# Optimization experiments

Measured on AMD Instinct MI355X. Metric: run time of the kernel, lower is better.

## Reference

```python
import jax, jax.numpy as jnp
import numpy as np

NUM_HEADS = 4
NUM_GROUPS = 8
EPS = 1e-5


def group_norm(x, w, b):
    # x: [B, C, H, W], 8 groups, per-channel affine
    B, C, H, W = x.shape
    g = x.reshape(B, NUM_GROUPS, C // NUM_GROUPS, H, W)
    mu = g.mean(axis=(2, 3, 4), keepdims=True)
    var = g.var(axis=(2, 3, 4), keepdims=True)
    g = (g - mu) * jax.lax.rsqrt(var + EPS)
    x = g.reshape(B, C, H, W)
    return x * w[None, :, None, None] + b[None, :, None, None]


def setup_inputs() -> dict:
    key = jax.random.key(0)
    ks = jax.random.split(key, 7)
    B, C, H, W = 16, 256, 32, 32
    x = jax.random.normal(ks[0], (B, C, H, W), dtype=jnp.float32)
    norm_w = jnp.ones((C,), jnp.float32)
    norm_b = jnp.zeros((C,), jnp.float32)
    # 1x1 convs == channel matmuls; fan-in scaled init
    qkv_w = jax.random.normal(ks[1], (3 * C, C), dtype=jnp.float32) / np.sqrt(C)
    qkv_b = jnp.zeros((3 * C,), jnp.float32)
    proj_w = jax.random.normal(ks[2], (C, C), dtype=jnp.float32) / np.sqrt(C)
    proj_b = jnp.zeros((C,), jnp.float32)
    return {"x": x, "norm_w": norm_w, "norm_b": norm_b,
            "qkv_w": qkv_w, "qkv_b": qkv_b,
            "proj_w": proj_w, "proj_b": proj_b}


def reference(x, norm_w, norm_b, qkv_w, qkv_b, proj_w, proj_b):
    B, C, H, W = x.shape
    nh = NUM_HEADS
    d = C // nh
    N = H * W

    h = group_norm(x, norm_w, norm_b)
    # 1x1 conv -> channel matmul: [B, 3C, H, W]
    qkv = jnp.einsum('oc,bchw->bohw', qkv_w, h) + qkv_b[None, :, None, None]
    qkv = qkv.reshape(B, 3, nh, d, N)
    q, k, v = qkv[:, 0], qkv[:, 1], qkv[:, 2]  # [B, nh, d, N]

    scale = d ** (-0.5)
    attn = jnp.einsum('bhcn,bhcm->bhnm', q, k) * scale  # [B, nh, N, N]
    attn = jax.nn.softmax(attn, axis=-1)
    out = jnp.einsum('bhnm,bhcm->bhcn', attn, v)  # [B, nh, d, N]
    out = out.reshape(B, C, H, W)
    out = jnp.einsum('oc,bchw->bohw', proj_w, out) + proj_b[None, :, None, None]
    return x + out
```

## Files before the change

kernel.cpp:

```cpp
#include <hip/hip_runtime.h>
#include <math.h>

#define BATCH 16
#define CH 256
#define NG 8
#define NH 4
#define HD 64
#define NN 1024
#define GSZ 32
#define GELEMS (GSZ * NN)

typedef __attribute__((ext_vector_type(8))) __bf16 bf16x8;
typedef __attribute__((ext_vector_type(4))) __bf16 bf16x4;
typedef __attribute__((ext_vector_type(4))) _Float16 f16x4;
typedef __attribute__((ext_vector_type(4))) float f32x4;

__device__ __forceinline__ unsigned short f2b(float f) {
    union { __bf16 h; unsigned short u; } c; c.h = (__bf16)f; return c.u;
}
__device__ __forceinline__ unsigned short f2h(float f) {
    union { _Float16 h; unsigned short u; } c; c.h = (_Float16)f; return c.u;
}

#define MFMA(a, b, c) __builtin_amdgcn_mfma_f32_16x16x32_bf16(a, b, c, 0, 0, 0)
#define MFMA16(a, b, c) __builtin_amdgcn_mfma_f32_16x16x16f16(a, b, c, 0, 0, 0)

__global__ __launch_bounds__(256) void prep_kernel(
    const float* __restrict__ x, const float* __restrict__ qkv_w,
    const float* __restrict__ proj_w, float* __restrict__ stats,
    unsigned short* __restrict__ wq, unsigned short* __restrict__ wp)
{
    int tid = threadIdx.x;
    if (blockIdx.x >= 128) {
        int t = (blockIdx.x - 128) * 256 + tid;
        const float* src; unsigned short* dst; size_t off;
        if (t < 24576) { src = qkv_w; dst = wq; off = (size_t)t * 8; }
        else           { src = proj_w; dst = wp; off = (size_t)(t - 24576) * 8; }
        const float4* s4 = (const float4*)(src + off);
        float4 a = s4[0], b = s4[1];
        bf16x8 pk;
        pk[0] = (__bf16)a.x; pk[1] = (__bf16)a.y; pk[2] = (__bf16)a.z; pk[3] = (__bf16)a.w;
        pk[4] = (__bf16)b.x; pk[5] = (__bf16)b.y; pk[6] = (__bf16)b.z; pk[7] = (__bf16)b.w;
        *(bf16x8*)(dst + off) = pk;
        return;
    }
    int b = blockIdx.x >> 3, g = blockIdx.x & 7;
    const float4* x4 = (const float4*)(x + ((size_t)b * CH + g * GSZ) * NN);
    float s = 0.f, ss = 0.f;
    #pragma unroll
    for (int i = 0; i < 32; ++i) {
        float4 v = x4[tid + i * 256];
        s  += v.x + v.y + v.z + v.w;
        ss += v.x * v.x + v.y * v.y + v.z * v.z + v.w * v.w;
    }
    #pragma unroll
    for (int off = 1; off < 64; off <<= 1) {
        s  += __shfl_xor(s, off);
        ss += __shfl_xor(ss, off);
    }
    __shared__ float red[8];
    int wave = tid >> 6, lane = tid & 63;
    if (lane == 0) { red[wave] = s; red[4 + wave] = ss; }
    __syncthreads();
    if (tid == 0) {
        float ts  = red[0] + red[1] + red[2] + red[3];
        float tss = red[4] + red[5] + red[6] + red[7];
        float mu  = ts * (1.f / GELEMS);
        float var = tss * (1.f / GELEMS) - mu * mu;
        stats[blockIdx.x * 2] = mu;
        stats[blockIdx.x * 2 + 1] = rsqrtf(var + 1e-5f);
    }
}

__global__ __launch_bounds__(256) void gn_apply_kernel(
    const float* __restrict__ x, const float* __restrict__ w,
    const float* __restrict__ bb, const float* __restrict__ stats,
    unsigned short* __restrict__ hT)
{
    __shared__ float Ts[64][68];
    __shared__ float wcp[256], bcp[256];
    const int b = blockIdx.y, n0 = blockIdx.x * 64;
    const int tid = threadIdx.x;
    {
        int c = tid, g = c >> 5;
        float mu = stats[(b * 8 + g) * 2], rs = stats[(b * 8 + g) * 2 + 1];
        float wc = w[c] * rs;
        wcp[c] = wc; bcp[c] = bb[c] - mu * wc;
    }
    __syncthreads();
    const float* xb = x + (size_t)b * CH * NN;
    const int c_l = tid >> 2, nq = tid & 3;
    const int n_l = tid >> 2, cq = tid & 3;
    for (int cb = 0; cb < 4; ++cb) {
        #pragma unroll
        for (int i = 0; i < 4; ++i)
            *(float4*)&Ts[c_l][nq * 4 + i * 16] =
                *(const float4*)(xb + (size_t)(cb * 64 + c_l) * NN + n0 + nq * 4 + i * 16);
        __syncthreads();
        #pragma unroll
        for (int s = 0; s < 2; ++s) {
            int cbase = cq * 16 + s * 8;
            bf16x8 pk;
            #pragma unroll
            for (int j = 0; j < 8; ++j) {
                int c = cb * 64 + cbase + j;
                pk[j] = (__bf16)(Ts[cbase + j][n_l] * wcp[c] + bcp[c]);
            }
            *(bf16x8*)(hT + ((size_t)b * NN + n0 + n_l) * CH + cb * 64 + cbase) = pk;
        }
        __syncthreads();
    }
}

template <int KIND>
__global__ __launch_bounds__(256) void gemm_kernel(
    const unsigned short* __restrict__ AT,
    const unsigned short* __restrict__ Wb,
    const float* __restrict__ bias,
    unsigned short* __restrict__ outT, unsigned short* __restrict__ outV,
    const float* __restrict__ res, float* __restrict__ out)
{
    __shared__ __align__(16) unsigned short Ws[64][136];
    __shared__ __align__(16) unsigned short Hs[64][136];
    const int b = blockIdx.z, o0 = blockIdx.y * 64, n0 = blockIdx.x * 64;
    const int tid = threadIdx.x;
    const int lane = tid & 63, wv = tid >> 6;
    const int l = lane & 15, quad = lane >> 4;
    const int iw = wv & 1, jw = wv >> 1;
    const bool qk_mode = (KIND == 0) && (blockIdx.y < 8);
    const bool v_mode  = (KIND == 0) && (blockIdx.y >= 8);
    const int r4 = tid >> 2, c4 = tid & 3;

    f32x4 acc[2][2] = {};
    for (int st = 0; st < 2; ++st) {
        const int cc0 = st * 128;
        #pragma unroll
        for (int i = 0; i < 4; ++i) {
            int ch = c4 + i * 4;
            *(bf16x8*)&Ws[r4][ch * 8] =
                *(const bf16x8*)(Wb + (size_t)(o0 + r4) * CH + cc0 + ch * 8);
            *(bf16x8*)&Hs[r4][ch * 8] =
                *(const bf16x8*)(AT + ((size_t)b * NN + n0 + r4) * CH + cc0 + ch * 8);
        }
        __syncthreads();
        #pragma unroll
        for (int kt = 0; kt < 4; ++kt) {
            bf16x8 af[2], bf[2];
            #pragma unroll
            for (int i = 0; i < 2; ++i)
                af[i] = *(const bf16x8*)&Hs[iw * 32 + i * 16 + l][kt * 32 + quad * 8];
            #pragma unroll
            for (int j = 0; j < 2; ++j)
                bf[j] = *(const bf16x8*)&Ws[jw * 32 + j * 16 + l][kt * 32 + quad * 8];
            #pragma unroll
            for (int i = 0; i < 2; ++i)
                #pragma unroll
                for (int j = 0; j < 2; ++j)
                    acc[i][j] = v_mode ? MFMA(af[i], bf[j], acc[i][j])
                                       : MFMA(bf[j], af[i], acc[i][j]);
        }
        __syncthreads();
    }

    unsigned short* Cs = (unsigned short*)Ws;
    if (qk_mode) {
        #pragma unroll
        for (int i = 0; i < 2; ++i)
            #pragma unroll
            for (int j = 0; j < 2; ++j) {
                int o_p = jw * 32 + j * 16 + quad * 4;
                int n_l = iw * 32 + i * 16 + l;
                bf16x4 pk;
                #pragma unroll
                for (int r = 0; r < 4; ++r)
                    pk[r] = (__bf16)(acc[i][j][r] + bias[o0 + o_p + r]);
                *(bf16x4*)&Cs[n_l * 72 + o_p] = pk;
            }
        __syncthreads();
        int rr = tid >> 2, ch = tid & 3;
        bf16x8 a0 = *(const bf16x8*)&Cs[rr * 72 + ch * 16];
        bf16x8 a1 = *(const bf16x8*)&Cs[rr * 72 + ch * 16 + 8];
        unsigned short* dst = outT + ((size_t)b * NN + n0 + rr) * 512 + o0 + ch * 16;
        *(bf16x8*)dst = a0;
        *(bf16x8*)(dst + 8) = a1;
    } else if (v_mode) {
        #pragma unroll
        for (int i = 0; i < 2; ++i)
            #pragma unroll
            for (int j = 0; j < 2; ++j) {
                int n_p = iw * 32 + i * 16 + quad * 4;
                int o_l = jw * 32 + j * 16 + l;
                float bs = bias[o0 + o_l];
                f16x4 pk;
                #pragma unroll
                for (int r = 0; r < 4; ++r)
                    pk[r] = (_Float16)(acc[i][j][r] + bs);
                *(f16x4*)&Cs[o_l * 72 + n_p] = pk;
            }
        __syncthreads();
        int rr = tid >> 2, ch = tid & 3;
        bf16x8 a0 = *(const bf16x8*)&Cs[rr * 72 + ch * 16];
        bf16x8 a1 = *(const bf16x8*)&Cs[rr * 72 + ch * 16 + 8];
        unsigned short* dst = outV + ((size_t)b * CH + (o0 + rr - 512)) * NN + n0 + ch * 16;
        *(bf16x8*)dst = a0;
        *(bf16x8*)(dst + 8) = a1;
    } else {
        #pragma unroll
        for (int i = 0; i < 2; ++i)
            #pragma unroll
            for (int j = 0; j < 2; ++j) {
                int o = o0 + jw * 32 + j * 16 + quad * 4;
                int n = n0 + iw * 32 + i * 16 + l;
                #pragma unroll
                for (int r = 0; r < 4; ++r) {
                    size_t idx = ((size_t)b * CH + o + r) * NN + n;
                    out[idx] = acc[i][j][r] + bias[o + r] + res[idx];
                }
            }
    }
}

__global__ __launch_bounds__(256, 3) void attn_kernel(
    const unsigned short* __restrict__ qkvT,
    const unsigned short* __restrict__ vbuf,
    unsigned short* __restrict__ ctxT)
{
    __shared__ __align__(16) unsigned short KV[2][8192];
    __shared__ float Lred[2][32];
    const int id = blockIdx.x;
    const int bh = id & 63, nt = id >> 6;
    const int b = bh >> 2, hh = bh & 3;
    const int n0 = nt * 64;
    const int tid = threadIdx.x;
    const int lane = tid & 63, w = tid >> 6;
    const int l = lane & 15, quad = lane >> 4;
    const int qx = w & 1, ky = w >> 1;
    const float KL2E = 0.125f * 1.44269504f;
    const int r4 = tid >> 2, c4 = tid & 3;

    bf16x8 qf[2][2];
    {
        const unsigned short* qp = qkvT + ((size_t)b * NN + n0 + 32 * qx + l) * 512 + hh * 64;
        #pragma unroll
        for (int ns = 0; ns < 2; ++ns)
            #pragma unroll
            for (int kt = 0; kt < 2; ++kt)
                qf[ns][kt] = *(const bf16x8*)(qp + (size_t)ns * 16 * 512 + kt * 32 + quad * 8);
    }

    const unsigned short* gk = qkvT + ((size_t)b * NN + r4) * 512 + 256 + hh * 64;
    const unsigned short* gv = vbuf + ((size_t)b * CH + hh * 64 + r4) * NN;
    const int p0 = (c4 ^ (r4 & 7)) * 8, p1 = ((c4 + 4) ^ (r4 & 7)) * 8;

    bf16x8 kpre0, kpre1, vpre0, vpre1;
    kpre0 = *(const bf16x8*)(gk + c4 * 8);
    kpre1 = *(const bf16x8*)(gk + (c4 + 4) * 8);
    vpre0 = *(const bf16x8*)(gv + c4 * 8);
    vpre1 = *(const bf16x8*)(gv + (c4 + 4) * 8);
    *(bf16x8*)&KV[0][r4 * 64 + p0] = kpre0;
    *(bf16x8*)&KV[0][r4 * 64 + p1] = kpre1;
    *(bf16x8*)&KV[0][4096 + r4 * 64 + p0] = vpre0;
    *(bf16x8*)&KV[0][4096 + r4 * 64 + p1] = vpre1;
    __syncthreads();

    float l_w[2] = {0.f, 0.f};
    f32x4 oacc[2][4] = {};

    for (int mt = 0; mt < 16; ++mt) {
        const int cur = mt & 1;
        if (mt < 15) {
            const unsigned short* gk1 = gk + (size_t)(mt + 1) * 64 * 512;
            const unsigned short* gv1 = gv + (mt + 1) * 64;
            kpre0 = *(const bf16x8*)(gk1 + c4 * 8);
            kpre1 = *(const bf16x8*)(gk1 + (c4 + 4) * 8);
            vpre0 = *(const bf16x8*)(gv1 + c4 * 8);
            vpre1 = *(const bf16x8*)(gv1 + (c4 + 4) * 8);
        }

        bf16x8 kf[2][2];
        #pragma unroll
        for (int mt2 = 0; mt2 < 2; ++mt2)
            #pragma unroll
            for (int kt = 0; kt < 2; ++kt)
                kf[mt2][kt] = *(const bf16x8*)
                    &KV[cur][(32 * ky + 16 * mt2 + l) * 64 + (((kt * 4 + quad) ^ (l & 7)) * 8)];

        f32x4 sacc[2][2] = {};
        #pragma unroll
        for (int kt = 0; kt < 2; ++kt)
            #pragma unroll
            for (int mt2 = 0; mt2 < 2; ++mt2)
                #pragma unroll
                for (int ns = 0; ns < 2; ++ns)
                    sacc[mt2][ns] = MFMA(kf[mt2][kt], qf[ns][kt], sacc[mt2][ns]);

        f16x4 pf[2][2];
        #pragma unroll
        for (int mt2 = 0; mt2 < 2; ++mt2)
            #pragma unroll
            for (int ns = 0; ns < 2; ++ns)
                #pragma unroll
                for (int r = 0; r < 4; ++r) {
                    float p = exp2f(sacc[mt2][ns][r] * KL2E);
                    l_w[ns] += p;
                    pf[mt2][ns][r] = (_Float16)p;
                }

        #pragma unroll
        for (int mt2 = 0; mt2 < 2; ++mt2) {
            const int q8 = 4 * ky + 2 * mt2 + (quad >> 1);
            const int vo = ((q8 ^ (l & 7)) * 8) + (quad & 1) * 4;
            #pragma unroll
            for (int ct = 0; ct < 4; ++ct) {
                f16x4 va = *(const f16x4*)&KV[cur][4096 + (16 * ct + l) * 64 + vo];
                #pragma unroll
                for (int ns = 0; ns < 2; ++ns)
                    oacc[ns][ct] = MFMA16(va, pf[mt2][ns], oacc[ns][ct]);
            }
        }

        if (mt < 15) {
            const int nxt = cur ^ 1;
            *(bf16x8*)&KV[nxt][r4 * 64 + p0] = kpre0;
            *(bf16x8*)&KV[nxt][r4 * 64 + p1] = kpre1;
            *(bf16x8*)&KV[nxt][4096 + r4 * 64 + p0] = vpre0;
            *(bf16x8*)&KV[nxt][4096 + r4 * 64 + p1] = vpre1;
            __syncthreads();
        }
    }

    #pragma unroll
    for (int ns = 0; ns < 2; ++ns) {
        l_w[ns] += __shfl_xor(l_w[ns], 16);
        l_w[ns] += __shfl_xor(l_w[ns], 32);
    }
    float* Ored = (float*)&KV[0][0];
    if (ky == 1) {
        #pragma unroll
        for (int ns = 0; ns < 2; ++ns) {
            if (quad == 0) Lred[qx][ns * 16 + l] = l_w[ns];
            #pragma unroll
            for (int ct = 0; ct < 4; ++ct)
                #pragma unroll
                for (int r = 0; r < 4; ++r)
                    Ored[qx * 2048 + (16 * ct + quad * 4 + r) * 32 + ns * 16 + l] =
                        oacc[ns][ct][r];
        }
    }
    __syncthreads();
    if (ky == 0) {
        unsigned short* cb = ctxT + ((size_t)b * NN + n0 + 32 * qx) * CH + hh * 64;
        #pragma unroll
        for (int ns = 0; ns < 2; ++ns) {
            float inv = 1.f / (l_w[ns] + Lred[qx][ns * 16 + l]);
            #pragma unroll
            for (int ct = 0; ct < 4; ++ct) {
                bf16x4 pk;
                #pragma unroll
                for (int r = 0; r < 4; ++r)
                    pk[r] = (__bf16)((oacc[ns][ct][r] +
                             Ored[qx * 2048 + (16 * ct + quad * 4 + r) * 32 + ns * 16 + l]) * inv);
                *(bf16x4*)(cb + (size_t)(ns * 16 + l) * CH + 16 * ct + quad * 4) = pk;
            }
        }
    }
}

extern "C" void kernel_launch(void* const* d_in, const int* in_sizes, int n_in,
                              void* d_out, int out_size, void* d_ws, size_t ws_size,
                              hipStream_t stream)
{
    const float* x      = (const float*)d_in[0];
    const float* norm_w = (const float*)d_in[1];
    const float* norm_b = (const float*)d_in[2];
    const float* qkv_w  = (const float*)d_in[3];
    const float* qkv_b  = (const float*)d_in[4];
    const float* proj_w = (const float*)d_in[5];
    const float* proj_b = (const float*)d_in[6];
    float* out = (float*)d_out;

    unsigned short* hT   = (unsigned short*)d_ws;
    unsigned short* qkvT = hT   + (size_t)BATCH * NN * CH;
    unsigned short* vbuf = qkvT + (size_t)BATCH * NN * 512;
    unsigned short* ctxT = vbuf + (size_t)BATCH * CH * NN;
    unsigned short* wq   = ctxT + (size_t)BATCH * NN * CH;
    unsigned short* wp   = wq + (size_t)768 * CH;
    float* stats         = (float*)(wp + (size_t)CH * CH);

    prep_kernel<<<dim3(256), 256, 0, stream>>>(x, qkv_w, proj_w, stats, wq, wp);
    gn_apply_kernel<<<dim3(16, BATCH), 256, 0, stream>>>(x, norm_w, norm_b, stats, hT);
    gemm_kernel<0><<<dim3(NN / 64, 12, BATCH), 256, 0, stream>>>(
        hT, wq, qkv_b, qkvT, vbuf, nullptr, nullptr);
    attn_kernel<<<dim3(1024), 256, 0, stream>>>(qkvT, vbuf, ctxT);
    gemm_kernel<1><<<dim3(NN / 64, 4, BATCH), 256, 0, stream>>>(
        ctxT, wp, proj_b, nullptr, nullptr, x, out);
}
```

Baseline: 146.6 us.

## Fuse group-norm stats and apply into one kernel, raise attention occupancy

Merges the group-norm statistics kernel and the apply/transpose kernel into a single kernel where each block computes stats for one (batch, group) and then normalizes and transposes that group's 32 channels to bf16. This removes one launch and the stats round trip, and the group's data is likely still in cache for the second pass. It also raises the attention kernel's launch-bounds min-blocks from 3 to 4, which may force register spills. The fused apply phase uses only 128 blocks with narrower writes, which may lower parallelism.

New measurement: 145.8 us. About the same (-0.5%).

```diff
diff --git a/kernel.cpp b/kernel.cpp
--- a/kernel.cpp
+++ b/kernel.cpp
@@ -25,9 +25,10 @@
 #define MFMA(a, b, c) __builtin_amdgcn_mfma_f32_16x16x32_bf16(a, b, c, 0, 0, 0)
 #define MFMA16(a, b, c) __builtin_amdgcn_mfma_f32_16x16x16f16(a, b, c, 0, 0, 0)
 
-__global__ __launch_bounds__(256) void prep_kernel(
-    const float* __restrict__ x, const float* __restrict__ qkv_w,
-    const float* __restrict__ proj_w, float* __restrict__ stats,
+__global__ __launch_bounds__(256) void gnw_kernel(
+    const float* __restrict__ x, const float* __restrict__ w,
+    const float* __restrict__ bb, const float* __restrict__ qkv_w,
+    const float* __restrict__ proj_w, unsigned short* __restrict__ hT,
     unsigned short* __restrict__ wq, unsigned short* __restrict__ wp)
 {
     int tid = threadIdx.x;
@@ -44,8 +45,10 @@
         *(bf16x8*)(dst + off) = pk;
         return;
     }
-    int b = blockIdx.x >> 3, g = blockIdx.x & 7;
-    const float4* x4 = (const float4*)(x + ((size_t)b * CH + g * GSZ) * NN);
+    const int b = blockIdx.x >> 3, g = blockIdx.x & 7;
+    const float* xb = x + ((size_t)b * CH + g * GSZ) * NN;
+    const float4* x4 = (const float4*)xb;
+
     float s = 0.f, ss = 0.f;
     #pragma unroll
     for (int i = 0; i < 32; ++i) {
@@ -67,47 +70,33 @@
         float tss = red[4] + red[5] + red[6] + red[7];
         float mu  = ts * (1.f / GELEMS);
         float var = tss * (1.f / GELEMS) - mu * mu;
-        stats[blockIdx.x * 2] = mu;
-        stats[blockIdx.x * 2 + 1] = rsqrtf(var + 1e-5f);
-    }
-}
-
-__global__ __launch_bounds__(256) void gn_apply_kernel(
-    const float* __restrict__ x, const float* __restrict__ w,
-    const float* __restrict__ bb, const float* __restrict__ stats,
-    unsigned short* __restrict__ hT)
-{
-    __shared__ float Ts[64][68];
-    __shared__ float wcp[256], bcp[256];
-    const int b = blockIdx.y, n0 = blockIdx.x * 64;
-    const int tid = threadIdx.x;
-    {
-        int c = tid, g = c >> 5;
-        float mu = stats[(b * 8 + g) * 2], rs = stats[(b * 8 + g) * 2 + 1];
-        float wc = w[c] * rs;
-        wcp[c] = wc; bcp[c] = bb[c] - mu * wc;
+        red[0] = mu; red[1] = rsqrtf(var + 1e-5f);
     }
     __syncthreads();
-    const float* xb = x + (size_t)b * CH * NN;
-    const int c_l = tid >> 2, nq = tid & 3;
-    const int n_l = tid >> 2, cq = tid & 3;
-    for (int cb = 0; cb < 4; ++cb) {
-        #pragma unroll
-        for (int i = 0; i < 4; ++i)
-            *(float4*)&Ts[c_l][nq * 4 + i * 16] =
-                *(const float4*)(xb + (size_t)(cb * 64 + c_l) * NN + n0 + nq * 4 + i * 16);
-        __syncthreads();
-        #pragma unroll
-        for (int s = 0; s < 2; ++s) {
-            int cbase = cq * 16 + s * 8;
-            bf16x8 pk;
-            #pragma unroll
-            for (int j = 0; j < 8; ++j) {
-                int c = cb * 64 + cbase + j;
-                pk[j] = (__bf16)(Ts[cbase + j][n_l] * wcp[c] + bcp[c]);
-            }
-            *(bf16x8*)(hT + ((size_t)b * NN + n0 + n_l) * CH + cb * 64 + cbase) = pk;
-        }
+    const float mu = red[0], rs = red[1];
+
+    const int co = tid & 3;
+    float wcv[8], bcv[8];
+    #pragma unroll
+    for (int j = 0; j < 8; ++j) {
+        int c = g * GSZ + co * 8 + j;
+        wcv[j] = w[c] * rs;
+        bcv[j] = bb[c] - mu * wcv[j];
+    }
+    __shared__ float Ts[32][66];
+    const int cs = tid >> 3, q = tid & 7;
+    const int n_l = tid >> 2;
+    for (int nt = 0; nt < 16; ++nt) {
+        const float2* src = (const float2*)(xb + (size_t)cs * NN + nt * 64 + q * 8);
+        #pragma unroll
+        for (int t = 0; t < 4; ++t)
+            *(float2*)&Ts[cs][q * 8 + t * 2] = src[t];
+        __syncthreads();
+        bf16x8 pk;
+        #pragma unroll
+        for (int j = 0; j < 8; ++j)
+            pk[j] = (__bf16)(Ts[co * 8 + j][n_l] * wcv[j] + bcv[j]);
+        *(bf16x8*)(hT + ((size_t)b * NN + nt * 64 + n_l) * CH + g * GSZ + co * 8) = pk;
         __syncthreads();
     }
 }
@@ -220,7 +209,7 @@
     }
 }
 
-__global__ __launch_bounds__(256, 3) void attn_kernel(
+__global__ __launch_bounds__(256, 4) void attn_kernel(
     const unsigned short* __restrict__ qkvT,
     const unsigned short* __restrict__ vbuf,
     unsigned short* __restrict__ ctxT)
@@ -385,10 +374,8 @@
     unsigned short* ctxT = vbuf + (size_t)BATCH * CH * NN;
     unsigned short* wq   = ctxT + (size_t)BATCH * NN * CH;
     unsigned short* wp   = wq + (size_t)768 * CH;
-    float* stats         = (float*)(wp + (size_t)CH * CH);
-
-    prep_kernel<<<dim3(256), 256, 0, stream>>>(x, qkv_w, proj_w, stats, wq, wp);
-    gn_apply_kernel<<<dim3(16, BATCH), 256, 0, stream>>>(x, norm_w, norm_b, stats, hT);
+
+    gnw_kernel<<<dim3(256), 256, 0, stream>>>(x, norm_w, norm_b, qkv_w, proj_w, hT, wq, wp);
     gemm_kernel<0><<<dim3(NN / 64, 12, BATCH), 256, 0, stream>>>(
         hT, wq, qkv_b, qkvT, vbuf, nullptr, nullptr);
     attn_kernel<<<dim3(1024), 256, 0, stream>>>(qkvT, vbuf, ctxT);
```
